# Kernel tuning notes

Measured on AMD Instinct MI355X. Metric: run time of the kernel, lower is better.

## Reference

```python
import jax, jax.numpy as jnp
import numpy as np

D = 4          # subsample stride for quantized refs
R = 6          # local search radius
P = 2 * R + 1  # 13
N = P * P      # 169
C = 32         # one-hot classes
BETA = 50.0
SIG = 1.0      # gaussian kernel sigma for kernel_soft_argmax
MPR = 12       # memory_patch_R
MPP = 2 * MPR + 1  # 25
DIL_INT = 15


def bilinear_gather(img, ys, xs):
    # img (b,c,h,w); ys,xs (b,n,h,w) float pixel coords; zero padding outside.
    b, c, h, w = img.shape
    y0f = jnp.floor(ys); x0f = jnp.floor(xs)
    wy = ys - y0f; wx = xs - x0f
    y0 = y0f.astype(jnp.int32); x0 = x0f.astype(jnp.int32)
    imgf = img.reshape(b, c, h * w)

    def corner(yi, xi, wgt):
        valid = (yi >= 0) & (yi < h) & (xi >= 0) & (xi < w)
        idx = jnp.clip(yi, 0, h - 1) * w + jnp.clip(xi, 0, w - 1)  # (b,n,h,w)
        g = jax.vmap(lambda f, ix: f[:, ix])(imgf, idx)            # (b,c,n,h,w)
        return g * (wgt * valid)[:, None]

    return (corner(y0, x0, (1 - wy) * (1 - wx))
            + corner(y0, x0 + 1, (1 - wy) * wx)
            + corner(y0 + 1, x0, wy * (1 - wx))
            + corner(y0 + 1, x0 + 1, wy * wx))


def deform_im2col(img, offset):
    # img (b,c,h,w); offset (b,h,w,2) ordered (dx,dy); returns (b,c,N,h,w)
    b, c, h, w = img.shape
    n = jnp.arange(N)
    dy = (n // P - R).astype(jnp.float32)
    dx = (n % P - R).astype(jnp.float32)
    yy = jnp.arange(h, dtype=jnp.float32)[:, None]
    xx = jnp.arange(w, dtype=jnp.float32)[None, :]
    ys = yy[None, None] + offset[..., 1][:, None] + dy[None, :, None, None]
    xs = xx[None, None] + offset[..., 0][:, None] + dx[None, :, None, None]
    return bilinear_gather(img, ys, xs)


def local_corr(t, r, rad, dil):
    # SpatialCorrelationSampler(kernel_size=1, patch_size=2*rad+1, dilation_patch=dil)
    pad = rad * dil
    rp = jnp.pad(r, ((0, 0), (0, 0), (pad, pad), (pad, pad)))
    offs = jnp.arange(2 * rad + 1) * dil

    def dot(oy, ox):
        rs = jax.lax.dynamic_slice(rp, (0, 0, oy, ox), t.shape)
        return jnp.sum(t * rs, axis=1)  # (b,h,w)

    f = jax.vmap(lambda oy: jax.vmap(lambda ox: dot(oy, ox))(offs))(offs)  # (Pp,Pp,b,h,w)
    return jnp.transpose(f, (2, 0, 1, 3, 4))  # (b,Pp,Pp,h,w), axis1=dy, axis2=dx


def unfold(x, ksz, pad):
    # torch F.unfold: (b,c,h,w) -> (b,c,ksz*ksz,h*w), n = ky*ksz+kx, zero pad
    b, c, h, w = x.shape
    xp = jnp.pad(x, ((0, 0), (0, 0), (pad, pad), (pad, pad)))
    offs = jnp.arange(ksz)
    sl = jax.vmap(lambda oy: jax.vmap(
        lambda ox: jax.lax.dynamic_slice(xp, (0, 0, oy, ox), x.shape))(offs))(offs)
    return jnp.transpose(sl, (2, 3, 0, 1, 4, 5)).reshape(b, c, ksz * ksz, h * w)


def kernel_soft_argmax(corr):
    # corr (B, N, h, w): gaussian-weight then softmax(beta * .) over N
    k = jnp.arange(P, dtype=jnp.float32)
    ctr = (P - 1) / 2.0
    g = jnp.exp(-(((k[None, :] - ctr) ** 2) + ((k[:, None] - ctr) ** 2)) / (2 * SIG ** 2))
    return jax.nn.softmax(BETA * (g.reshape(1, N, 1, 1) * corr), axis=1)


def get_grid(corr):
    # corr (B, N, h, w) -> soft-argmax grid (B, h, w, 2) in normalized coords
    B, n, h, w = corr.shape
    # replicate the torch meshgrid variable swap in the original get_grid
    x_map = jnp.broadcast_to(jnp.linspace(-1.0, 1.0, w)[None, :], (h, w)).astype(jnp.float32)
    y_map = jnp.broadcast_to(jnp.linspace(-1.0, 1.0, h)[:, None], (h, w)).astype(jnp.float32)
    xg = unfold(x_map[None, None], P, R)[:, 0]  # (1,N,hw)
    yg = unfold(y_map[None, None], P, R)[:, 0]
    wgt = corr.reshape(B, n, h * w)
    wgt = wgt / jnp.sum(wgt, 1, keepdims=True)
    gx = (wgt * xg).sum(1).reshape(B, h, w, 1)
    gy = (wgt * yg).sum(1).reshape(B, h, w, 1)
    return jnp.concatenate([gx, gy], 3)


def forward(feats_r, feats_t, quantized_r, ref_index, current_ind):
    ref_list = [int(v) for v in np.asarray(ref_index)]  # static config
    cur = int(current_ind)
    nref = feats_r.shape[0]
    nsearch = len([x for x in ref_list if cur - x > DIL_INT])
    dirates = [min(4, (cur - x) // DIL_INT + 1) for x in ref_list if cur - x > DIL_INT]
    b, c, h, w = feats_t.shape

    mdy = jnp.arange(-MPR, MPR + 1, dtype=jnp.float32)
    corrs, offsets = [], []
    for si in range(nsearch):
        cc = local_corr(feats_t, feats_r[si], MPR, dirates[si])       # (b,25,25,h,w)
        cc = jax.nn.softmax(cc.reshape(b, MPP * MPP, h * w), axis=1)
        cc = cc.reshape(b, MPP, MPP, h, w)
        offx = jnp.einsum('bpqhw,q->bhw', cc, mdy)   # expectation of dx
        offy = jnp.einsum('bpqhw,p->bhw', cc, mdy)   # expectation of dy
        off = jnp.stack([offx, offy], -1) * float(dirates[si])        # (b,h,w,2)
        offsets.append(off)
        col0 = deform_im2col(feats_r[si], off)                        # (b,c,N,h,w)
        corrs.append(jnp.einsum('bchw,bcnhw->bnhw', feats_t, col0))
    for ind in range(nsearch, nref):
        corrs.append(local_corr(feats_t, feats_r[ind], R, 1).reshape(b, N, h, w))

    corr = jnp.concatenate(corrs, 0)                 # (b*nref, N, h, w)
    corr = kernel_soft_argmax(corr)
    corr = corr.reshape(b, 1, N * nref, h * w)
    grid = get_grid(corr.reshape(-1, N, h, w))       # (b*nref, h, w, 2)

    # prep: subsample ::D and one-hot single-channel label maps
    labels = quantized_r[:, :, 0, ::D, ::D]          # (nref, b, h, w)
    qr = (labels[:, :, None] == jnp.arange(C)[None, None, :, None, None]).astype(jnp.float32)

    cols = []
    for i in range(nsearch):
        cols.append(deform_im2col(qr[i], offsets[i]).reshape(b, C, N, h * w))
    for i in range(nsearch, nref):
        cols.append(unfold(qr[i], P, R))
    image_uf = jnp.concatenate(cols, 2)              # (b, C, N*nref, hw)

    out = jnp.einsum('bnl,bcnl->bcl', corr[:, 0], image_uf).reshape(b, C, h, w)
    return out, grid


def setup_inputs() -> dict:
    key = jax.random.key(0)
    k1, k2, k3 = jax.random.split(key, 3)
    feats_r = jax.random.normal(k1, (3, 1, 64, 64, 64), dtype=jnp.float32)
    feats_t = jax.random.normal(k2, (1, 64, 64, 64), dtype=jnp.float32)
    quantized_r = jax.random.randint(k3, (3, 1, 1, 256, 256), 0, C, dtype=jnp.int32)
    return {
        'feats_r': feats_r,
        'feats_t': feats_t,
        'quantized_r': quantized_r,
        'ref_index': np.arange(3),
        'current_ind': 16,
    }


def reference(feats_r, feats_t, quantized_r, ref_index, current_ind):
    return forward(feats_r, feats_t, quantized_r, ref_index, current_ind)
```

## Files before the change

### kernel.cpp

```cpp
#include <hip/hip_runtime.h>


#define NPIX 4096

__device__ __forceinline__ float pdot(float4 t0, float4 t1, float4 t2,
                                      float4 t3, float4 a, float4 b, float4 c,
                                      float4 d) {
  float s0 = 0.f, s1 = 0.f, s2 = 0.f, s3 = 0.f;
  s0 = fmaf(t0.x, a.x, s0); s1 = fmaf(t0.y, a.y, s1);
  s2 = fmaf(t0.z, a.z, s2); s3 = fmaf(t0.w, a.w, s3);
  s0 = fmaf(t1.x, b.x, s0); s1 = fmaf(t1.y, b.y, s1);
  s2 = fmaf(t1.z, b.z, s2); s3 = fmaf(t1.w, b.w, s3);
  s0 = fmaf(t2.x, c.x, s0); s1 = fmaf(t2.y, c.y, s1);
  s2 = fmaf(t2.z, c.z, s2); s3 = fmaf(t2.w, c.w, s3);
  s0 = fmaf(t3.x, d.x, s0); s1 = fmaf(t3.y, d.y, s1);
  s2 = fmaf(t3.z, d.z, s2); s3 = fmaf(t3.w, d.w, s3);
  return (s0 + s1) + (s2 + s3);
}

__device__ __forceinline__ float xpose_reduce4(float p0, float p1, float p2,
                                               float p3, int tx) {
  bool o1 = tx & 1, o2 = tx & 2;
  float x01 = __shfl_xor(o1 ? p0 : p1, 1);
  float x23 = __shfl_xor(o1 ? p2 : p3, 1);
  float sA = (o1 ? p1 : p0) + x01;
  float sB = (o1 ? p3 : p2) + x23;
  float z = __shfl_xor(o2 ? sA : sB, 2);
  return o2 ? (sB + z) : (sA + z);
}

__device__ __forceinline__ float wredmax(float v) {
#pragma unroll
  for (int o = 32; o; o >>= 1) v = fmaxf(v, __shfl_down(v, o));
  return __shfl(v, 0);
}
__device__ __forceinline__ float wredsum(float v) {
#pragma unroll
  for (int o = 32; o; o >>= 1) v += __shfl_down(v, o);
  return __shfl(v, 0);
}

__global__ __launch_bounds__(256) void k_transpose(
    const float* __restrict__ ft, const float* __restrict__ fr,
    const int* __restrict__ q, float* __restrict__ tT, float* __restrict__ rT,
    unsigned char* __restrict__ lblp) {
  __shared__ float tile[64][65];
  int img = blockIdx.y;
  int pixBase = blockIdx.x * 64;
  const float* src = (img == 0) ? ft : fr + (img - 1) * (64 * NPIX);
  float* dst = (img == 0) ? tT : rT + (img - 1) * (64 * NPIX);
  int tid = threadIdx.x;
#pragma unroll
  for (int it = 0; it < 4; ++it) {
    int idx = it * 256 + tid;
    int c = idx >> 4;
    int p4 = (idx & 15) << 2;
    float4 v = *(const float4*)&src[c * NPIX + pixBase + p4];
    tile[p4 + 0][c] = v.x;
    tile[p4 + 1][c] = v.y;
    tile[p4 + 2][c] = v.z;
    tile[p4 + 3][c] = v.w;
  }
  __syncthreads();
#pragma unroll
  for (int it = 0; it < 4; ++it) {
    int idx = it * 256 + tid;
    int p = idx >> 4;
    int c4 = (idx & 15) << 2;
    float4 v = make_float4(tile[p][c4], tile[p][c4 + 1], tile[p][c4 + 2],
                           tile[p][c4 + 3]);
    *(float4*)&dst[(pixBase + p) * 64 + c4] = v;
  }
  if (img >= 1 && tid < 64) {
    int pix = pixBase + tid;
    lblp[(img - 1) * 4096 + pix] = (unsigned char)
        q[(img - 1) * 65536 + (pix >> 6) * 1024 + (pix & 63) * 4];
  }
}

__global__ __launch_bounds__(512) void k_fused(
    const float* __restrict__ tT, const float* __restrict__ rT,
    const unsigned char* __restrict__ lblp, float* __restrict__ out,
    float* __restrict__ grid) {
  int xg = blockIdx.x, y = blockIdx.y;
  int x0 = (xg >> 1) * 8 + (xg & 1);
  int tid = threadIdx.x;
  int gg = tid >> 2, tx = tid & 3;
  int w = tid >> 6, lane = tid & 63;
  int p = w & 3, h = w >> 2;

  __shared__ __align__(16) float tlds[4][64];
  __shared__ float ccf[2500];
  __shared__ float offs[4][2];
  __shared__ float bins[4][33];
  __shared__ float wred[8][4];

  if (tid < 132) ((float*)bins)[tid] = 0.f;
  if (tid < 64) {
    int pp = tid >> 4, c4 = tid & 15;
    ((float4*)&tlds[pp][0])[c4] =
        ((const float4*)&tT[((y << 6) + x0 + 2 * pp) << 6])[c4];
  }
  __syncthreads();

  const float4* TL0 = (const float4*)&tlds[0][0];
  const float4* TL1 = (const float4*)&tlds[1][0];
  const float4* TL2 = (const float4*)&tlds[2][0];
  const float4* TL3 = (const float4*)&tlds[3][0];

  {
    int u = gg & 31;
    int rx = x0 - 24 + 2 * u;
    bool col_ok = ((unsigned)rx < 64u) & (u < 28);
    int colB = min(max(rx, 0), 63) * 64 + tx * 4;
    int ox = u - tx;
    bool st_col = (unsigned)ox < 25u;
    int oyb = gg >> 5;
#pragma unroll 1
    for (int r = 0; r < 7; ++r) {
      int oy = oyb + 4 * r;
      int ry = y + 2 * oy - 24;
      bool ok = col_ok & (oy < 25) & ((unsigned)ry < 64u);
      const float4* rp = (const float4*)&rT[min(max(ry, 0), 63) * 4096 + colB];
      float4 ra = rp[0], rb = rp[4], rc = rp[8], rd = rp[12];
      float p0 = pdot(TL0[tx], TL0[tx + 4], TL0[tx + 8], TL0[tx + 12], ra, rb, rc, rd);
      float p1 = pdot(TL1[tx], TL1[tx + 4], TL1[tx + 8], TL1[tx + 12], ra, rb, rc, rd);
      float p2 = pdot(TL2[tx], TL2[tx + 4], TL2[tx + 8], TL2[tx + 12], ra, rb, rc, rd);
      float p3 = pdot(TL3[tx], TL3[tx + 4], TL3[tx + 8], TL3[tx + 12], ra, rb, rc, rd);
      float v = xpose_reduce4(p0, p1, p2, p3, tx);
      v = ok ? v : 0.f;
      if (st_col && (oy < 25)) ccf[tx * 625 + oy * 25 + ox] = v;
    }
  }
  __syncthreads();

  {
    float vv[5];
    float m = -3e38f;
#pragma unroll
    for (int it = 0; it < 5; ++it) {
      int o = lane + (h << 6) + (it << 7);
      float v = (o < 625) ? ccf[p * 625 + o] : -3e38f;
      vv[it] = v;
      m = fmaxf(m, v);
    }
    m = wredmax(m);
    float s = 0.f, sx = 0.f, sy = 0.f;
#pragma unroll
    for (int it = 0; it < 5; ++it) {
      int o = lane + (h << 6) + (it << 7);
      int oy = o / 25, ox = o - oy * 25;
      float e = __expf(vv[it] - m);
      s += e;
      sx += e * (float)(ox - 12);
      sy += e * (float)(oy - 12);
    }
    s = wredsum(s); sx = wredsum(sx); sy = wredsum(sy);
    if (lane == 0) {
      wred[w][0] = m; wred[w][1] = s; wred[w][2] = sx; wred[w][3] = sy;
    }
    __syncthreads();
    if (h == 0 && lane == 0) {
      float m2 = wred[w + 4][0], s2 = wred[w + 4][1];
      float sx2 = wred[w + 4][2], sy2 = wred[w + 4][3];
      float M = fmaxf(m, m2);
      float f1 = __expf(m - M), f2 = __expf(m2 - M);
      float S = s * f1 + s2 * f2;
      offs[p][0] = 2.f * (sx * f1 + sx2 * f2) / S;
      offs[p][1] = 2.f * (sy * f1 + sy2 * f2) / S;
    }
  }
  __syncthreads();

  {
    int pp = gg >> 5;
    float offx = offs[pp][0], offy = offs[pp][1];
    int iy0 = y + (int)floorf(offy) - 6;
    int ix0 = x0 + 2 * pp + (int)floorf(offx) - 6;
    const float4* TL = (const float4*)&tlds[pp][0];
    float4 T0 = TL[tx], T1 = TL[tx + 4], T2 = TL[tx + 8], T3 = TL[tx + 12];
    int ib = gg & 31;
#pragma unroll 1
    for (int r = 0; r < 7; ++r) {
      int idx = ib + (r << 5);
      int a = idx / 14, b = idx - a * 14;
      int ry = iy0 + a, rx = ix0 + b;
      bool ok = (idx < 196) & ((unsigned)ry < 64u) & ((unsigned)rx < 64u);
      const float4* rp = (const float4*)
          &rT[(min(max(ry, 0), 63) * 64 + min(max(rx, 0), 63)) * 64];
      float4 ra = rp[tx], rb = rp[tx + 4], rc = rp[tx + 8], rd = rp[tx + 12];
      float v = pdot(T0, T1, T2, T3, ra, rb, rc, rd);
      v += __shfl_xor(v, 1);
      v += __shfl_xor(v, 2);
      v = ok ? v : 0.f;
      if ((idx < 196) && tx == 0) ccf[pp * 196 + idx] = v;
    }
  }
  __syncthreads();

  {
    int px = x0 + 2 * p;
    int pix = y * 64 + px;
    float offx = offs[p][0], offy = offs[p][1];
    float fy = floorf(offy), fx = floorf(offx);
    float wy = offy - fy, wx = offx - fx;
    float w00 = (1.f - wy) * (1.f - wx), w01 = (1.f - wy) * wx;
    float w10 = wy * (1.f - wx), w11 = wy * wx;
    const float* Dw = &ccf[p * 196];
    float sc[2];
    float m = -3e38f;
#pragma unroll
    for (int it = 0; it < 2; ++it) {
      int o = lane + (h << 6) + (it << 7);
      float scv = -3e38f;
      if (o < 169) {
        int i = o / 13, j = o - i * 13;
        float v = w00 * Dw[i * 14 + j] + w01 * Dw[i * 14 + j + 1] +
                  w10 * Dw[(i + 1) * 14 + j] + w11 * Dw[(i + 1) * 14 + j + 1];
        float di = (float)((i - 6) * (i - 6) + (j - 6) * (j - 6));
        scv = 50.f * __expf(-0.5f * di) * v;
      }
      sc[it] = scv;
      m = fmaxf(m, scv);
    }
    m = wredmax(m);
    float ee[2];
    float s = 0.f, gx = 0.f, gy = 0.f;
#pragma unroll
    for (int it = 0; it < 2; ++it) {
      int o = lane + (h << 6) + (it << 7);
      int i = o / 13, j = o - i * 13;
      float e = __expf(sc[it] - m);
      ee[it] = e;
      int yy = y + i - 6, xx = px + j - 6;
      bool inb = (o < 169) && (unsigned)yy < 64u && (unsigned)xx < 64u;
      float xgv = inb ? (-1.f + (2.f / 63.f) * (float)xx) : 0.f;
      float ygv = inb ? (-1.f + (2.f / 63.f) * (float)yy) : 0.f;
      s += e;
      gx += e * xgv;
      gy += e * ygv;
    }
    s = wredsum(s); gx = wredsum(gx); gy = wredsum(gy);
    if (lane == 0) {
      wred[w][0] = m; wred[w][1] = s; wred[w][2] = gx; wred[w][3] = gy;
    }
    __syncthreads();
    float mo = wred[w ^ 4][0], so = wred[w ^ 4][1];
    float gxo = wred[w ^ 4][2], gyo = wred[w ^ 4][3];
    float M = fmaxf(m, mo);
    float fs = __expf(m - M), fo = __expf(mo - M);
    float invS = 1.f / (s * fs + so * fo);
#pragma unroll
    for (int it = 0; it < 2; ++it) {
      int o = lane + (h << 6) + (it << 7);
      if (o < 169) ccf[1024 + p * 169 + o] = ee[it] * fs * invS;
    }
    if (h == 0 && lane == 0) {
      grid[pix * 2 + 0] = (gx * fs + gxo * fo) * invS;
      grid[pix * 2 + 1] = (gy * fs + gyo * fo) * invS;
    }
  }
  __syncthreads();

  {
    float offx = offs[p][0], offy = offs[p][1];
    float fy = floorf(offy), fx = floorf(offx);
    float wy = offy - fy, wx = offx - fx;
    float w00 = (1.f - wy) * (1.f - wx), w01 = (1.f - wy) * wx;
    float w10 = wy * (1.f - wx), w11 = wy * wx;
    int by = y + (int)fy - 6, bx = x0 + 2 * p + (int)fx - 6;
    const float* crp = &ccf[1024 + p * 169];
#pragma unroll
    for (int it = 0; it < 2; ++it) {
      int idx = lane + (h << 6) + (it << 7);
      if (idx < 196) {
        int a = idx / 14, b = idx - a * 14;
        int ry = by + a, rx = bx + b;
        if ((unsigned)ry < 64u && (unsigned)rx < 64u) {
          float wgt = 0.f;
          if (a < 13) {
            if (b < 13) wgt = fmaf(w00, crp[a * 13 + b], wgt);
            if (b > 0) wgt = fmaf(w01, crp[a * 13 + b - 1], wgt);
          }
          if (a > 0) {
            if (b < 13) wgt = fmaf(w10, crp[(a - 1) * 13 + b], wgt);
            if (b > 0) wgt = fmaf(w11, crp[(a - 1) * 13 + b - 1], wgt);
          }
          if (wgt != 0.f) atomicAdd(&bins[p][lblp[ry * 64 + rx]], wgt);
        }
      }
    }
  }

#pragma unroll 1
  for (int k = 1; k <= 2; ++k) {
    const float* rb0 = rT + k * (64 * NPIX);
    {
#pragma unroll 1
      for (int r = 0; r < 2; ++r) {
        int tu = gg + (r << 7);
        int i = tu / 19, u = tu - i * 19;
        int ry = y + i - 6, rx = x0 - 6 + u;
        bool ok = (i < 13) & ((unsigned)ry < 64u) & ((unsigned)rx < 64u);
        const float4* rp = (const float4*)
            &rb0[(min(max(ry, 0), 63) * 64 + min(max(rx, 0), 63)) * 64];
        float4 ra = rp[tx], rb = rp[tx + 4], rc = rp[tx + 8], rd = rp[tx + 12];
        float p0 = pdot(TL0[tx], TL0[tx + 4], TL0[tx + 8], TL0[tx + 12], ra, rb, rc, rd);
        float p1 = pdot(TL1[tx], TL1[tx + 4], TL1[tx + 8], TL1[tx + 12], ra, rb, rc, rd);
        float p2 = pdot(TL2[tx], TL2[tx + 4], TL2[tx + 8], TL2[tx + 12], ra, rb, rc, rd);
        float p3 = pdot(TL3[tx], TL3[tx + 4], TL3[tx + 8], TL3[tx + 12], ra, rb, rc, rd);
        float v = xpose_reduce4(p0, p1, p2, p3, tx);
        v = ok ? v : 0.f;
        int j = u - 2 * tx;
        if ((i < 13) && ((unsigned)j < 13u)) ccf[tx * 169 + i * 13 + j] = v;
      }
    }
    __syncthreads();
    {
      int px = x0 + 2 * p;
      int pix = y * 64 + px;
      float sc[2];
      float m = -3e38f;
#pragma unroll
      for (int it = 0; it < 2; ++it) {
        int o = lane + (h << 6) + (it << 7);
        float scv = -3e38f;
        if (o < 169) {
          int i = o / 13, j = o - i * 13;
          float di = (float)((i - 6) * (i - 6) + (j - 6) * (j - 6));
          scv = 50.f * __expf(-0.5f * di) * ccf[p * 169 + o];
        }
        sc[it] = scv;
        m = fmaxf(m, scv);
      }
      m = wredmax(m);
      float ee[2];
      float s = 0.f, gx = 0.f, gy = 0.f;
#pragma unroll
      for (int it = 0; it < 2; ++it) {
        int o = lane + (h << 6) + (it << 7);
        int i = o / 13, j = o - i * 13;
        float e = __expf(sc[it] - m);
        ee[it] = e;
        int yy = y + i - 6, xx = px + j - 6;
        bool inb = (o < 169) && (unsigned)yy < 64u && (unsigned)xx < 64u;
        float xgv = inb ? (-1.f + (2.f / 63.f) * (float)xx) : 0.f;
        float ygv = inb ? (-1.f + (2.f / 63.f) * (float)yy) : 0.f;
        s += e;
        gx += e * xgv;
        gy += e * ygv;
      }
      s = wredsum(s); gx = wredsum(gx); gy = wredsum(gy);
      if (lane == 0) {
        wred[w][0] = m; wred[w][1] = s; wred[w][2] = gx; wred[w][3] = gy;
      }
      __syncthreads();
      float mo = wred[w ^ 4][0], so = wred[w ^ 4][1];
      float gxo = wred[w ^ 4][2], gyo = wred[w ^ 4][3];
      float M = fmaxf(m, mo);
      float fs = __expf(m - M), fo = __expf(mo - M);
      float invS = 1.f / (s * fs + so * fo);
#pragma unroll
      for (int it = 0; it < 2; ++it) {
        int o = lane + (h << 6) + (it << 7);
        if (o < 169) {
          int i = o / 13, j = o - i * 13;
          int yy = y + i - 6, xx = px + j - 6;
          if ((unsigned)yy < 64u && (unsigned)xx < 64u)
            atomicAdd(&bins[p][lblp[(k << 12) + yy * 64 + xx]],
                      ee[it] * fs * invS);
        }
      }
      if (h == 0 && lane == 0) {
        grid[(k * NPIX + pix) * 2 + 0] = (gx * fs + gxo * fo) * invS;
        grid[(k * NPIX + pix) * 2 + 1] = (gy * fs + gyo * fo) * invS;
      }
    }
  }
  __syncthreads();

  if (tid < 128) {
    int pp = tid & 3, c = tid >> 2;
    out[c * NPIX + y * 64 + x0 + 2 * pp] = bins[pp][c];
  }
}

extern "C" void kernel_launch(void* const* d_in, const int* in_sizes, int n_in,
                              void* d_out, int out_size, void* d_ws,
                              size_t ws_size, hipStream_t stream) {
  const float* fr = (const float*)d_in[0];
  const float* ft = (const float*)d_in[1];
  const int* q = (const int*)d_in[2];
  float* out = (float*)d_out;
  float* grid = out + 32 * NPIX;

  float* ws = (float*)d_ws;
  float* tT = ws;
  float* rT = ws + 262144;
  unsigned char* lblp = (unsigned char*)(ws + 1048576);

  k_transpose<<<dim3(64, 4), 256, 0, stream>>>(ft, fr, q, tT, rT, lblp);
  k_fused<<<dim3(16, 64), 512, 0, stream>>>(tT, rT, lblp, out, grid);
}
```

Measured before the change: 55.25 us.

## Split channel dot products across 8 lanes and keep target features in registers

The correlation phases now spread each 64-channel dot product over 8 lanes with 8 channels each instead of 4 lanes with 16, which halves the per-thread FMA and load work per iteration and doubles the iteration count. The target feature vectors are loaded straight from global memory into registers rather than staged through a shared-memory tile, which removes one barrier and the LDS reads. The launch bounds now request 8 waves per SIMD. In exchange the butterfly reduction gains an extra shuffle stage, and half the lanes do redundant work that is never stored.

```diff
diff --git a/kernel.cpp b/kernel.cpp
--- a/kernel.cpp
+++ b/kernel.cpp
@@ -3,30 +3,37 @@
 
 #define NPIX 4096
 
-__device__ __forceinline__ float pdot(float4 t0, float4 t1, float4 t2,
-                                      float4 t3, float4 a, float4 b, float4 c,
-                                      float4 d) {
-  float s0 = 0.f, s1 = 0.f, s2 = 0.f, s3 = 0.f;
-  s0 = fmaf(t0.x, a.x, s0); s1 = fmaf(t0.y, a.y, s1);
-  s2 = fmaf(t0.z, a.z, s2); s3 = fmaf(t0.w, a.w, s3);
-  s0 = fmaf(t1.x, b.x, s0); s1 = fmaf(t1.y, b.y, s1);
-  s2 = fmaf(t1.z, b.z, s2); s3 = fmaf(t1.w, b.w, s3);
-  s0 = fmaf(t2.x, c.x, s0); s1 = fmaf(t2.y, c.y, s1);
-  s2 = fmaf(t2.z, c.z, s2); s3 = fmaf(t2.w, c.w, s3);
-  s0 = fmaf(t3.x, d.x, s0); s1 = fmaf(t3.y, d.y, s1);
-  s2 = fmaf(t3.z, d.z, s2); s3 = fmaf(t3.w, d.w, s3);
+__device__ __forceinline__ float pdot8(float4 t0, float4 t1, float4 a,
+                                       float4 b) {
+  float s0 = t0.x * a.x, s1 = t0.y * a.y, s2 = t0.z * a.z, s3 = t0.w * a.w;
+  s0 = fmaf(t1.x, b.x, s0);
+  s1 = fmaf(t1.y, b.y, s1);
+  s2 = fmaf(t1.z, b.z, s2);
+  s3 = fmaf(t1.w, b.w, s3);
   return (s0 + s1) + (s2 + s3);
 }
 
-__device__ __forceinline__ float xpose_reduce4(float p0, float p1, float p2,
-                                               float p3, int tx) {
-  bool o1 = tx & 1, o2 = tx & 2;
+__device__ __forceinline__ float red8_4(float p0, float p1, float p2,
+                                        float p3, int tx) {
+  p0 += __shfl_xor(p0, 4);
+  p1 += __shfl_xor(p1, 4);
+  p2 += __shfl_xor(p2, 4);
+  p3 += __shfl_xor(p3, 4);
+  int t2 = tx & 3;
+  bool o1 = t2 & 1, o2 = t2 & 2;
   float x01 = __shfl_xor(o1 ? p0 : p1, 1);
   float x23 = __shfl_xor(o1 ? p2 : p3, 1);
   float sA = (o1 ? p1 : p0) + x01;
   float sB = (o1 ? p3 : p2) + x23;
   float z = __shfl_xor(o2 ? sA : sB, 2);
   return o2 ? (sB + z) : (sA + z);
+}
+
+__device__ __forceinline__ float red8(float v) {
+  v += __shfl_xor(v, 1);
+  v += __shfl_xor(v, 2);
+  v += __shfl_xor(v, 4);
+  return v;
 }
 
 __device__ __forceinline__ float wredmax(float v) {
@@ -78,58 +85,52 @@
   }
 }
 
-__global__ __launch_bounds__(512) void k_fused(
+#define LT8(N, XC)                                                         \
+  const float4* tp##N = (const float4*)&tT[((y << 6) + (XC)) << 6];        \
+  float4 t##N##0 = tp##N[2 * tx], t##N##1 = tp##N[2 * tx + 1];
+
+__global__ __launch_bounds__(512, 8) void k_fused(
     const float* __restrict__ tT, const float* __restrict__ rT,
     const unsigned char* __restrict__ lblp, float* __restrict__ out,
     float* __restrict__ grid) {
   int xg = blockIdx.x, y = blockIdx.y;
   int x0 = (xg >> 1) * 8 + (xg & 1);
   int tid = threadIdx.x;
-  int gg = tid >> 2, tx = tid & 3;
+  int g8 = tid >> 3, tx = tid & 7;
   int w = tid >> 6, lane = tid & 63;
   int p = w & 3, h = w >> 2;
 
-  __shared__ __align__(16) float tlds[4][64];
   __shared__ float ccf[2500];
   __shared__ float offs[4][2];
   __shared__ float bins[4][33];
   __shared__ float wred[8][4];
 
   if (tid < 132) ((float*)bins)[tid] = 0.f;
-  if (tid < 64) {
-    int pp = tid >> 4, c4 = tid & 15;
-    ((float4*)&tlds[pp][0])[c4] =
-        ((const float4*)&tT[((y << 6) + x0 + 2 * pp) << 6])[c4];
-  }
-  __syncthreads();
-
-  const float4* TL0 = (const float4*)&tlds[0][0];
-  const float4* TL1 = (const float4*)&tlds[1][0];
-  const float4* TL2 = (const float4*)&tlds[2][0];
-  const float4* TL3 = (const float4*)&tlds[3][0];
 
   {
-    int u = gg & 31;
+    LT8(0, x0 + 0) LT8(1, x0 + 2) LT8(2, x0 + 4) LT8(3, x0 + 6)
+    int u = g8 & 31;
+    int oyb = g8 >> 5;
     int rx = x0 - 24 + 2 * u;
     bool col_ok = ((unsigned)rx < 64u) & (u < 28);
-    int colB = min(max(rx, 0), 63) * 64 + tx * 4;
-    int ox = u - tx;
-    bool st_col = (unsigned)ox < 25u;
-    int oyb = gg >> 5;
-#pragma unroll 1
-    for (int r = 0; r < 7; ++r) {
-      int oy = oyb + 4 * r;
+    int colB = min(max(rx, 0), 63) * 64 + tx * 8;
+    int pst = tx & 3;
+    int ox = u - pst;
+    bool st = (tx < 4) & ((unsigned)ox < 25u);
+#pragma unroll 2
+    for (int r = 0; r < 13; ++r) {
+      int oy = oyb + 2 * r;
       int ry = y + 2 * oy - 24;
       bool ok = col_ok & (oy < 25) & ((unsigned)ry < 64u);
       const float4* rp = (const float4*)&rT[min(max(ry, 0), 63) * 4096 + colB];
-      float4 ra = rp[0], rb = rp[4], rc = rp[8], rd = rp[12];
-      float p0 = pdot(TL0[tx], TL0[tx + 4], TL0[tx + 8], TL0[tx + 12], ra, rb, rc, rd);
-      float p1 = pdot(TL1[tx], TL1[tx + 4], TL1[tx + 8], TL1[tx + 12], ra, rb, rc, rd);
-      float p2 = pdot(TL2[tx], TL2[tx + 4], TL2[tx + 8], TL2[tx + 12], ra, rb, rc, rd);
-      float p3 = pdot(TL3[tx], TL3[tx + 4], TL3[tx + 8], TL3[tx + 12], ra, rb, rc, rd);
-      float v = xpose_reduce4(p0, p1, p2, p3, tx);
+      float4 ra = rp[0], rb = rp[1];
+      float p0 = pdot8(t00, t01, ra, rb);
+      float p1 = pdot8(t10, t11, ra, rb);
+      float p2 = pdot8(t20, t21, ra, rb);
+      float p3 = pdot8(t30, t31, ra, rb);
+      float v = red8_4(p0, p1, p2, p3, tx);
       v = ok ? v : 0.f;
-      if (st_col && (oy < 25)) ccf[tx * 625 + oy * 25 + ox] = v;
+      if (st && (oy < 25)) ccf[pst * 625 + oy * 25 + ox] = v;
     }
   }
   __syncthreads();
@@ -173,27 +174,25 @@
   __syncthreads();
 
   {
-    int pp = gg >> 5;
+    int pp = g8 >> 4;
+    int ib = g8 & 15;
+    const float4* Tp = (const float4*)&tT[((y << 6) + x0 + 2 * pp) << 6];
+    float4 T0 = Tp[2 * tx], T1 = Tp[2 * tx + 1];
     float offx = offs[pp][0], offy = offs[pp][1];
     int iy0 = y + (int)floorf(offy) - 6;
     int ix0 = x0 + 2 * pp + (int)floorf(offx) - 6;
-    const float4* TL = (const float4*)&tlds[pp][0];
-    float4 T0 = TL[tx], T1 = TL[tx + 4], T2 = TL[tx + 8], T3 = TL[tx + 12];
-    int ib = gg & 31;
-#pragma unroll 1
-    for (int r = 0; r < 7; ++r) {
-      int idx = ib + (r << 5);
+#pragma unroll 2
+    for (int r = 0; r < 13; ++r) {
+      int idx = ib + (r << 4);
       int a = idx / 14, b = idx - a * 14;
       int ry = iy0 + a, rx = ix0 + b;
       bool ok = (idx < 196) & ((unsigned)ry < 64u) & ((unsigned)rx < 64u);
       const float4* rp = (const float4*)
           &rT[(min(max(ry, 0), 63) * 64 + min(max(rx, 0), 63)) * 64];
-      float4 ra = rp[tx], rb = rp[tx + 4], rc = rp[tx + 8], rd = rp[tx + 12];
-      float v = pdot(T0, T1, T2, T3, ra, rb, rc, rd);
-      v += __shfl_xor(v, 1);
-      v += __shfl_xor(v, 2);
-      v = ok ? v : 0.f;
-      if ((idx < 196) && tx == 0) ccf[pp * 196 + idx] = v;
+      float4 ra = rp[2 * tx], rb = rp[2 * tx + 1];
+      float q = pdot8(T0, T1, ra, rb);
+      q = red8(q);
+      if ((idx < 196) && tx == 0) ccf[pp * 196 + idx] = ok ? q : 0.f;
     }
   }
   __syncthreads();
@@ -296,23 +295,26 @@
   for (int k = 1; k <= 2; ++k) {
     const float* rb0 = rT + k * (64 * NPIX);
     {
-#pragma unroll 1
-      for (int r = 0; r < 2; ++r) {
-        int tu = gg + (r << 7);
-        int i = tu / 19, u = tu - i * 19;
+      LT8(0, x0 + 0) LT8(1, x0 + 2) LT8(2, x0 + 4) LT8(3, x0 + 6)
+#pragma unroll 2
+      for (int r = 0; r < 4; ++r) {
+        int idx = g8 + (r << 6);
+        int i = idx / 19, u = idx - i * 19;
         int ry = y + i - 6, rx = x0 - 6 + u;
         bool ok = (i < 13) & ((unsigned)ry < 64u) & ((unsigned)rx < 64u);
         const float4* rp = (const float4*)
             &rb0[(min(max(ry, 0), 63) * 64 + min(max(rx, 0), 63)) * 64];
-        float4 ra = rp[tx], rb = rp[tx + 4], rc = rp[tx + 8], rd = rp[tx + 12];
-        float p0 = pdot(TL0[tx], TL0[tx + 4], TL0[tx + 8], TL0[tx + 12], ra, rb, rc, rd);
-        float p1 = pdot(TL1[tx], TL1[tx + 4], TL1[tx + 8], TL1[tx + 12], ra, rb, rc, rd);
-        float p2 = pdot(TL2[tx], TL2[tx + 4], TL2[tx + 8], TL2[tx + 12], ra, rb, rc, rd);
-        float p3 = pdot(TL3[tx], TL3[tx + 4], TL3[tx + 8], TL3[tx + 12], ra, rb, rc, rd);
-        float v = xpose_reduce4(p0, p1, p2, p3, tx);
+        float4 ra = rp[2 * tx], rb = rp[2 * tx + 1];
+        float p0 = pdot8(t00, t01, ra, rb);
+        float p1 = pdot8(t10, t11, ra, rb);
+        float p2 = pdot8(t20, t21, ra, rb);
+        float p3 = pdot8(t30, t31, ra, rb);
+        float v = red8_4(p0, p1, p2, p3, tx);
         v = ok ? v : 0.f;
-        int j = u - 2 * tx;
-        if ((i < 13) && ((unsigned)j < 13u)) ccf[tx * 169 + i * 13 + j] = v;
+        int pst = tx & 3;
+        int j = u - 2 * pst;
+        if ((tx < 4) && (i < 13) && ((unsigned)j < 13u))
+          ccf[pst * 169 + i * 13 + j] = v;
       }
     }
     __syncthreads();
```

Measured after the change: 66.28 us. +20.0%, slower.
